# Optimization experiments

Hardware: AMD Instinct MI355X
Metric: run time of the kernel (lower is better)

The kernel has to match this reference:

```python
import jax, jax.numpy as jnp
import numpy as np
import math

B, T, D = 4, 2048, 1024
N, D_OUT = 1024, 1024
EPS_A = 1e-4
PROJ_BOUND = 1.0


def setup_inputs() -> dict:
    key = jax.random.key(0)
    ks = jax.random.split(key, 4)
    # reset_parameters: rho=0.99, delta0=1.0
    rho, delta0 = 0.99, 1.0
    alpha0 = -math.log(rho) / delta0
    alpha_log_val = math.log(math.expm1(alpha0))
    delta_bias_val = math.log(math.expm1(delta0))
    return {
        "u": jax.random.normal(ks[0], (B, T, D), dtype=jnp.float32),
        "z0": jnp.zeros((B, N), dtype=jnp.float32),
        "W_in_raw": 0.02 * jax.random.normal(ks[1], (N, D), dtype=jnp.float32),
        "W_out_raw": 0.02 * jax.random.normal(ks[2], (D_OUT, N), dtype=jnp.float32),
        "pn_w": 0.02 * jax.random.normal(ks[3], (3 * N, D), dtype=jnp.float32),
        "pn_b": jnp.zeros((3 * N,), dtype=jnp.float32),
        "alpha_log": jnp.full((N,), alpha_log_val, dtype=jnp.float32),
        "delta_bias": jnp.full((N,), delta_bias_val, dtype=jnp.float32),
        "log_gamma": jnp.float32(0.0),
    }


def _bounded_linear(x, W, bound):
    # y = x @ (W/scale)^T with ||W/scale||_2 <= bound (exact spectral norm)
    sigma = jnp.maximum(jnp.linalg.norm(W, ord=2), 1e-5)
    scale = jnp.maximum(sigma / bound, 1.0)
    return x @ (W / scale).T


def reference(u, z0, W_in_raw, W_out_raw, pn_w, pn_b, alpha_log, delta_bias, log_gamma):
    g = jnp.exp(log_gamma)
    u_scaled = g * _bounded_linear(u, W_in_raw, PROJ_BOUND)        # (B,T,N)
    raw = u @ pn_w.T + pn_b                                        # (B,T,3N)
    delta_raw, b_raw, c_raw = jnp.split(raw, 3, axis=-1)
    delta = jax.nn.softplus(delta_raw + delta_bias)
    alpha = jax.nn.softplus(alpha_log)                             # (N,)
    a = jnp.minimum(jnp.exp(-delta * alpha), 1.0 - EPS_A)          # (B,T,N)
    b = jnp.tanh(b_raw)
    c = jnp.tanh(c_raw)
    # exact spectral norm of [[a,b],[c,0]] per coordinate
    p = a * a + c * c
    r = b * b
    q = a * b
    disc = (p - r) * (p - r) + 4.0 * q * q
    lam_max = 0.5 * (p + r + jnp.sqrt(disc + 1e-12))
    sigma = jnp.sqrt(lam_max + 1e-12)
    scale = jnp.maximum(sigma, 1.0)
    a, b, c = a / scale, b / scale, c / scale
    # diagonal recurrence z_{t+1} = a_t * z_t + b_t * u_scaled_t via associative scan
    bu = b * u_scaled
    bu = bu.at[:, 0].add(a[:, 0] * z0)
    def combine(x, y):
        a1, b1 = x
        a2, b2 = y
        return (a2 * a1, a2 * b1 + b2)
    _, z_next = jax.lax.associative_scan(combine, (a, bu), axis=1)  # z_1..z_T (B,T,N)
    # y_t = W_out (c_t * z_t) with z_t = state BEFORE update (one-step delay)
    states = jnp.concatenate([z0[:, None, :], z_next[:, :-1, :]], axis=1)  # z_0..z_{T-1}
    y_hat = c * states
    y = _bounded_linear(y_hat, W_out_raw, PROJ_BOUND)              # (B,T,D_out)
    return y
```

## Files before the change

### kernel.cpp

```cpp
#include <hip/hip_runtime.h>
#include <stdint.h>

#define B_ 4
#define T_ 2048
#define D_ 1024
#define N_ 1024
#define TC 16
#define NCH (T_/TC)
#define SQN 6

typedef __attribute__((ext_vector_type(4))) float f32x4;
typedef __attribute__((ext_vector_type(8))) short bf16x8;
typedef __attribute__((ext_vector_type(4))) unsigned short us4;

__device__ __forceinline__ unsigned short f2bf(float f){
  unsigned int u = __float_as_uint(f);
  return (unsigned short)((u + 0x7fffu + ((u >> 16) & 1u)) >> 16);
}
__device__ __forceinline__ float bf2f(unsigned short h){
  return __uint_as_float(((unsigned int)h) << 16);
}

__device__ __forceinline__ float inv_scale(const float* __restrict__ sc, int z){
  float ll = 0.f, w = 1.f, t = 1.f;
  #pragma unroll
  for (int i = 0; i <= SQN; i++){
    t = sc[8 + 2*i + z];
    ll += w * __logf(t);
    w *= 0.5f;
  }
  float F = sc[8 + 2*(SQN+1) + z];
  ll += w * __logf(F / (t*t));
  float sig = fmaxf(__expf(0.5f * ll), 1e-5f);
  return 1.f / fmaxf(sig, 1.f);
}

#define U4    2097152
#define WIN4   262144
#define PNW4   786432
#define WOUT4  262144
#define CONV_BLOCKS ((U4 + WIN4 + PNW4 + WOUT4 + 255)/256)

__global__ void k_convert_all(const float* __restrict__ u, const float* __restrict__ Win,
                              const float* __restrict__ pnw, const float* __restrict__ Wout,
                              unsigned short* __restrict__ u16, unsigned short* __restrict__ Wcat16,
                              unsigned short* __restrict__ Wout16, float* __restrict__ sc){
  if (blockIdx.x == 0 && threadIdx.x < 64) sc[threadIdx.x] = 0.f;
  long i = (long)blockIdx.x * 256 + threadIdx.x;
  const float* src; long o; size_t didx; unsigned short* dbuf;
  if (i < U4){
    src = u; o = i; dbuf = u16; didx = (size_t)o;
  } else if (i < U4+WIN4){
    o = i - U4; src = Win;
    int n = (int)(o >> 8), c4 = (int)(o & 255);
    dbuf = Wcat16; didx = (size_t)(4*n)*256 + c4;
  } else if (i < U4+WIN4+PNW4){
    o = i - (U4+WIN4); src = pnw;
    int m = (int)(o >> 8), c4 = (int)(o & 255);
    int s = (m >> 10) + 1, n = m & 1023;
    dbuf = Wcat16; didx = (size_t)(4*n + s)*256 + c4;
  } else if (i < U4+WIN4+PNW4+WOUT4){
    o = i - (U4+WIN4+PNW4); src = Wout; dbuf = Wout16; didx = (size_t)o;
  } else return;
  float4 v = ((const float4*)src)[o];
  us4 w;
  w.x = f2bf(v.x); w.y = f2bf(v.y); w.z = f2bf(v.z); w.w = f2bf(v.w);
  ((us4*)dbuf)[didx] = w;
}

__device__ __forceinline__ void load_lds16(const unsigned short* g, unsigned short* l){
  __builtin_amdgcn_global_load_lds((const __attribute__((address_space(1))) void*)g,
                                   (__attribute__((address_space(3))) void*)l, 16, 0, 0);
}

template<int OUTBF16>
__global__ __launch_bounds__(256) void k_gemm(
    const unsigned short* __restrict__ A,
    const unsigned short* __restrict__ Bmat,
    void* __restrict__ C0,
    int M, int N, int K,
    const float* __restrict__ sc, int step)
{
  __shared__ alignas(16) unsigned short As[128*64];
  __shared__ alignas(16) unsigned short Bs[128*64];
  const int tid = threadIdx.x;
  const int wid = tid >> 6;
  const int lane = tid & 63;
  const int bn = blockIdx.x, bm = blockIdx.y;

  char* C = (char*)C0;
  float outscale = (step >= 0) ? inv_scale(sc, step) : 1.f;

  const int wr = wid >> 1, wc = wid & 1;
  const int rg = lane >> 3;
  const int cby = (lane & 7) << 4;
  const int srow0 = wid * 32;
  const int frow = lane & 15;
  const int kgrp = lane >> 4;

  const unsigned short* ap[4];
  const unsigned short* bp[4];
  unsigned short* adst[4];
  unsigned short* bdst[4];
  #pragma unroll
  for (int i = 0; i < 4; i++){
    int r = srow0 + i*8 + rg;
    int cb = cby ^ ((r & 7) << 4);
    ap[i] = A    + (size_t)(bm*128 + r)*K + (cb >> 1);
    bp[i] = Bmat + (size_t)(bn*128 + r)*K + (cb >> 1);
    adst[i] = As + (srow0 + i*8)*64;
    bdst[i] = Bs + (srow0 + i*8)*64;
  }

  int aoff[4][2], boff[4][2];
  #pragma unroll
  for (int m = 0; m < 4; m++){
    int r = wr*64 + m*16 + frow;
    #pragma unroll
    for (int kk = 0; kk < 2; kk++)
      aoff[m][kk] = r*128 + ((kk*64 + kgrp*16) ^ ((r & 7) << 4));
  }
  #pragma unroll
  for (int n2 = 0; n2 < 4; n2++){
    int r = wc*64 + n2*16 + frow;
    #pragma unroll
    for (int kk = 0; kk < 2; kk++)
      boff[n2][kk] = r*128 + ((kk*64 + kgrp*16) ^ ((r & 7) << 4));
  }

  f32x4 acc[4][4] = {};

  for (int kt = 0; kt < K; kt += 64){
    #pragma unroll
    for (int i = 0; i < 4; i++){
      load_lds16(ap[i], adst[i]);
      load_lds16(bp[i], bdst[i]);
      ap[i] += 64; bp[i] += 64;
    }
    __syncthreads();
    #pragma unroll
    for (int kk = 0; kk < 2; kk++){
      bf16x8 af[4], bfv[4];
      #pragma unroll
      for (int m = 0; m < 4; m++)
        af[m] = *(const bf16x8*)((const char*)As + aoff[m][kk]);
      #pragma unroll
      for (int n2 = 0; n2 < 4; n2++)
        bfv[n2] = *(const bf16x8*)((const char*)Bs + boff[n2][kk]);
      #pragma unroll
      for (int m = 0; m < 4; m++)
        #pragma unroll
        for (int n2 = 0; n2 < 4; n2++)
          acc[m][n2] = __builtin_amdgcn_mfma_f32_16x16x32_bf16(af[m], bfv[n2], acc[m][n2], 0, 0, 0);
    }
    __syncthreads();
  }

  const int row0 = bm*128 + wr*64;
  const int col0 = bn*128 + wc*64 + frow;
  #pragma unroll
  for (int m = 0; m < 4; m++){
    #pragma unroll
    for (int n2 = 0; n2 < 4; n2++){
      const int col = col0 + n2*16;
      const int rb = row0 + m*16 + kgrp*4;
      #pragma unroll
      for (int j = 0; j < 4; j++){
        float v = acc[m][n2][j] * outscale;
        if (OUTBF16) ((unsigned short*)C)[(size_t)(rb + j)*N + col] = f2bf(v);
        else         ((float*)C)[(size_t)(rb + j)*N + col] = v;
      }
    }
  }
}

__global__ __launch_bounds__(256) void k_sq(
    const unsigned short* __restrict__ A0, unsigned short* __restrict__ C0,
    const unsigned short* __restrict__ A1, unsigned short* __restrict__ C1,
    float* __restrict__ sc, int step)
{
  __shared__ alignas(16) unsigned short As0[64*128], Bs0[64*128];
  __shared__ alignas(16) unsigned short As1[64*128], Bs1[64*128];
  const int tid = threadIdx.x;
  const int wid = tid >> 6;
  const int lane = tid & 63;
  const int z = blockIdx.z;

  int x = blockIdx.x, bm = 0;
  while (x >= 16 - bm){ x -= 16 - bm; bm++; }
  const int bn = bm + x;

  const unsigned short* A = z ? A1 : A0;
  unsigned short* C = z ? C1 : C0;
  const size_t rs = (step == 0 && z == 0) ? 4096 : 1024;
  float outscale = 1.f;
  if (step > 0){ float t = sc[8 + (step-1)*2 + z]; outscale = 1.f/(t*t); }

  const int wr = wid >> 1, wc = wid & 1;
  const int frow = lane & 15;
  const int kgrp = lane >> 4;

  const int srl = lane >> 4;
  const int sgr = lane & 15;
  const int swzr = wid*4 + srl;
  const int scol_e = ((sgr ^ swzr) << 3);

  const size_t Arow = (size_t)bm * 64;
  const size_t Brow = (size_t)bn * 64;

  f32x4 acc[2][2] = {};

  auto stage = [&](unsigned short* as, unsigned short* bs, int t){
    const int kt = t * 128;
    #pragma unroll
    for (int i = 0; i < 4; i++){
      int r = i*16 + wid*4 + srl;
      load_lds16(A + (Arow + r)*rs + kt + scol_e, as + (i*16 + wid*4)*128);
      load_lds16(A + (Brow + r)*rs + kt + scol_e, bs + (i*16 + wid*4)*128);
    }
  };

  auto compute = [&](const unsigned short* as, const unsigned short* bs){
    #pragma unroll
    for (int ks = 0; ks < 4; ks++){
      const int kb = ks*64 + kgrp*16;
      bf16x8 af[2], bfv[2];
      #pragma unroll
      for (int m = 0; m < 2; m++){
        int r = wr*32 + m*16 + frow;
        af[m] = *(const bf16x8*)((const char*)as + r*256 + (kb ^ (frow << 4)));
      }
      #pragma unroll
      for (int n2 = 0; n2 < 2; n2++){
        int r = wc*32 + n2*16 + frow;
        bfv[n2] = *(const bf16x8*)((const char*)bs + r*256 + (kb ^ (frow << 4)));
      }
      #pragma unroll
      for (int m = 0; m < 2; m++)
        #pragma unroll
        for (int n2 = 0; n2 < 2; n2++)
          acc[m][n2] = __builtin_amdgcn_mfma_f32_16x16x32_bf16(af[m], bfv[n2], acc[m][n2], 0, 0, 0);
    }
  };

  stage(As0, Bs0, 0);
  __syncthreads();
  for (int t2 = 0; t2 < 8; t2 += 2){
    if (t2 + 1 < 8) stage(As1, Bs1, t2 + 1);
    compute(As0, Bs0);
    __syncthreads();
    if (t2 + 2 < 8) stage(As0, Bs0, t2 + 2);
    compute(As1, Bs1);
    __syncthreads();
  }

  const int row0 = bm*64 + wr*32;
  const int col0 = bn*64 + wc*32 + frow;
  float fr = 0.f;
  #pragma unroll
  for (int m = 0; m < 2; m++){
    #pragma unroll
    for (int n2 = 0; n2 < 2; n2++){
      const int col = col0 + n2*16;
      const int rb = row0 + m*16 + kgrp*4;
      us4 tw;
      #pragma unroll
      for (int j = 0; j < 4; j++){
        float v = acc[m][n2][j] * outscale;
        unsigned short h = f2bf(v);
        C[(size_t)(rb + j)*1024 + col] = h;
        tw[j] = h;
        fr += v*v;
      }
      if (bm != bn)
        *(us4*)(C + (size_t)col*1024 + rb) = tw;
    }
  }
  if (bm == bn && wr == wc){
    int j = frow - kgrp*4;
    if (j >= 0 && j < 4){
      float d = (acc[0][0][j] + acc[1][1][j]) * outscale;
      atomicAdd(&sc[8 + step*2 + z], d);
    }
  }
  if (step == SQN){
    if (bm != bn) fr *= 2.f;
    #pragma unroll
    for (int off = 32; off; off >>= 1) fr += __shfl_down(fr, off, 64);
    if (lane == 0) atomicAdd(&sc[8 + 2*(SQN+1) + z], fr);
  }
}

__device__ __forceinline__ float softplusf(float x){
  return (x > 0.f) ? (x + __logf(1.f + __expf(-x))) : __logf(1.f + __expf(x));
}
__device__ __forceinline__ float tanhfastf(float x){
  float e = __expf(2.f * x);
  return 1.f - 2.f/(e + 1.f);
}
__device__ __forceinline__ void abc_from(float pin, float draw, float braw, float craw,
    float alpha, float ginv, float& a_o, float& bu_o, float& c_o){
  float sp = softplusf(draw);
  float av = __expf(-sp * alpha);
  av = fminf(av, 1.f - 1e-4f);
  float bv = tanhfastf(braw);
  float cv = tanhfastf(craw);
  float p = av*av + cv*cv;
  float r = bv*bv;
  float q = av*bv;
  float pr = p - r;
  float disc = pr*pr + 4.f*q*q;
  float lam = 0.5f*(p + r + sqrtf(disc + 1e-12f));
  float inv = fminf(rsqrtf(lam + 1e-12f), 1.f);
  a_o = av * inv;
  c_o = cv * inv;
  bu_o = (bv * inv) * (pin * ginv);
}

__global__ __launch_bounds__(256) void k_pass1(
    const unsigned short* __restrict__ P,
    const float* __restrict__ alog, const float* __restrict__ dbias,
    const float* __restrict__ pnb, const float* __restrict__ lgam,
    const float* __restrict__ sc,
    float* __restrict__ Asum, float* __restrict__ Ssum)
{
  const int tid = threadIdx.x;
  const int n0 = tid*4;
  const int ch = blockIdx.x, b = blockIdx.y;
  const float ginv = __expf(lgam[0]) * inv_scale(sc, 0);
  float alpha[4], bd[4], bb[4], bc[4], A[4], S[4];
  #pragma unroll
  for (int j = 0; j < 4; j++){
    alpha[j] = softplusf(alog[n0+j]);
    bd[j] = dbias[n0+j] + pnb[n0+j];
    bb[j] = pnb[N_ + n0+j];
    bc[j] = pnb[2*N_ + n0+j];
    A[j] = 1.f; S[j] = 0.f;
  }
  const unsigned short* Pr = P + (size_t)(b*T_ + ch*TC) * 4096 + 4*n0;
  #pragma unroll 2
  for (int i = 0; i < TC; i++){
    bf16x8 e0 = *(const bf16x8*)Pr;
    bf16x8 e1 = *(const bf16x8*)(Pr + 8);
    #pragma unroll
    for (int j = 0; j < 4; j++){
      const bf16x8& e = (j < 2) ? e0 : e1;
      const int o = (j & 1)*4;
      float a, bu, c;
      abc_from(bf2f((unsigned short)e[o]),   bf2f((unsigned short)e[o+1]) + bd[j],
               bf2f((unsigned short)e[o+2]) + bb[j], bf2f((unsigned short)e[o+3]) + bc[j],
               alpha[j], ginv, a, bu, c);
      S[j] = fmaf(a, S[j], bu);
      A[j] *= a;
    }
    Pr += 4096;
  }
  const size_t idx = (size_t)(b*NCH + ch)*N_ + n0;
  #pragma unroll
  for (int j = 0; j < 4; j++){ Asum[idx+j] = A[j]; Ssum[idx+j] = S[j]; }
}

__global__ void k_pass2(const float* __restrict__ Asum, const float* __restrict__ Ssum,
                        const float* __restrict__ z0, float* __restrict__ Zent)
{
  const int n = blockIdx.x*256 + threadIdx.x;
  const int b = blockIdx.y;
  float z = z0[b*N_ + n];
  for (int ch = 0; ch < NCH; ch++){
    const size_t idx = (size_t)(b*NCH + ch)*N_ + n;
    Zent[idx] = z;
    z = fmaf(Asum[idx], z, Ssum[idx]);
  }
}

__global__ __launch_bounds__(256) void k_pass3(
    const unsigned short* __restrict__ P,
    const float* __restrict__ alog, const float* __restrict__ dbias,
    const float* __restrict__ pnb, const float* __restrict__ lgam,
    const float* __restrict__ sc, const float* __restrict__ Zent,
    unsigned short* __restrict__ yh)
{
  const int tid = threadIdx.x;
  const int n0 = tid*4;
  const int ch = blockIdx.x, b = blockIdx.y;
  const float ginv = __expf(lgam[0]) * inv_scale(sc, 0);
  float alpha[4], bd[4], bb[4], bc[4], z[4];
  #pragma unroll
  for (int j = 0; j < 4; j++){
    alpha[j] = softplusf(alog[n0+j]);
    bd[j] = dbias[n0+j] + pnb[n0+j];
    bb[j] = pnb[N_ + n0+j];
    bc[j] = pnb[2*N_ + n0+j];
  }
  const size_t zidx = (size_t)(b*NCH + ch)*N_ + n0;
  #pragma unroll
  for (int j = 0; j < 4; j++) z[j] = Zent[zidx+j];
  const unsigned short* Pr = P + (size_t)(b*T_ + ch*TC) * 4096 + 4*n0;
  unsigned short* Y = yh + (size_t)(b*T_ + ch*TC)*N_ + n0;
  #pragma unroll 2
  for (int i = 0; i < TC; i++){
    bf16x8 e0 = *(const bf16x8*)Pr;
    bf16x8 e1 = *(const bf16x8*)(Pr + 8);
    us4 ow;
    #pragma unroll
    for (int j = 0; j < 4; j++){
      const bf16x8& e = (j < 2) ? e0 : e1;
      const int o = (j & 1)*4;
      float a, bu, c;
      abc_from(bf2f((unsigned short)e[o]),   bf2f((unsigned short)e[o+1]) + bd[j],
               bf2f((unsigned short)e[o+2]) + bb[j], bf2f((unsigned short)e[o+3]) + bc[j],
               alpha[j], ginv, a, bu, c);
      float yv = c * z[j];
      z[j] = fmaf(a, z[j], bu);
      ow[j] = f2bf(yv);
    }
    *(us4*)Y = ow;
    Y += N_;
    Pr += 4096;
  }
}

extern "C" void kernel_launch(void* const* d_in, const int* in_sizes, int n_in,
                              void* d_out, int out_size, void* d_ws, size_t ws_size,
                              hipStream_t stream)
{
  const float* u    = (const float*)d_in[0];
  const float* z0   = (const float*)d_in[1];
  const float* Win  = (const float*)d_in[2];
  const float* Wout = (const float*)d_in[3];
  const float* pnw  = (const float*)d_in[4];
  const float* pnb  = (const float*)d_in[5];
  const float* alog = (const float*)d_in[6];
  const float* dbias= (const float*)d_in[7];
  const float* lgam = (const float*)d_in[8];

  char* ws = (char*)d_ws;
  size_t off = 0;
  auto alloc = [&](size_t bytes) -> void* {
    void* p = ws + off;
    off += (bytes + 255) & ~(size_t)255;
    return p;
  };
  float*          sc     = (float*)         alloc(1024);
  unsigned short* u16    = (unsigned short*)alloc((size_t)8192*1024*2);
  unsigned short* Wcat16 = (unsigned short*)alloc((size_t)4096*1024*2);
  unsigned short* Wout16 = (unsigned short*)alloc((size_t)1024*1024*2);
  unsigned short* P16    = (unsigned short*)alloc((size_t)8192*4096*2);
  unsigned short* yh16   = (unsigned short*)alloc((size_t)8192*1024*2);
  unsigned short* Hping  = (unsigned short*)alloc((size_t)2*1024*1024*2);
  unsigned short* Hpong  = (unsigned short*)alloc((size_t)2*1024*1024*2);
  float*          Asum   = (float*)alloc((size_t)B_*NCH*N_*4);
  float*          Ssum   = (float*)alloc((size_t)B_*NCH*N_*4);
  float*          Zent   = (float*)alloc((size_t)B_*NCH*N_*4);

  k_convert_all<<<CONV_BLOCKS, 256, 0, stream>>>(u, Win, pnw, Wout, u16, Wcat16, Wout16, sc);

  dim3 gsq(136, 1, 2);
  k_sq<<<gsq, 256, 0, stream>>>(Wcat16, Hping, Wout16, Hping + (size_t)1024*1024, sc, 0);
  unsigned short* hin = Hping;
  unsigned short* hout = Hpong;
  for (int s = 1; s <= SQN; s++){
    k_sq<<<gsq, 256, 0, stream>>>(hin, hout, hin + (size_t)1024*1024, hout + (size_t)1024*1024, sc, s);
    unsigned short* t = hin; hin = hout; hout = t;
  }

  dim3 g1(4096/128, 8192/128);
  k_gemm<1><<<g1, 256, 0, stream>>>(u16, Wcat16, P16, 8192, 4096, 1024, sc, -1);

  dim3 gp1(NCH, B_);
  k_pass1<<<gp1, 256, 0, stream>>>(P16, alog, dbias, pnb, lgam, sc, Asum, Ssum);
  dim3 gp2(N_/256, B_);
  k_pass2<<<gp2, 256, 0, stream>>>(Asum, Ssum, z0, Zent);
  k_pass3<<<gp1, 256, 0, stream>>>(P16, alog, dbias, pnb, lgam, sc, Zent, yh16);

  dim3 g2(1024/128, 8192/128);
  k_gemm<0><<<g2, 256, 0, stream>>>(yh16, Wout16, d_out, 8192, 1024, 1024, sc, 1);
}
```

Before: 290.6 us.

## Fuse gate nonlinearity and chunk scan summaries into projection GEMM epilogue

The projection GEMM epilogue now transposes MFMA accumulators with lane shuffles, computes a, b·u and c per element, and stores packed bf16 a/c plus fp32 bu. It also reduces 16-step chunk summaries (A, S) with cross-lane shuffles. The separate pass1/pass2/pass3 kernels become a single scan kernel that folds all earlier chunk summaries serially per chunk and then runs the recurrence. This removes the bf16 P intermediate being read twice and the repeated transcendental work, in exchange for a heavier GEMM epilogue and an O(NCH) prefix loop per block.

Result: no change. 290.3 us (-0.1%).

```diff
diff --git a/kernel.cpp b/kernel.cpp
--- a/kernel.cpp
+++ b/kernel.cpp
@@ -33,6 +33,32 @@
   ll += w * __logf(F / (t*t));
   float sig = fmaxf(__expf(0.5f * ll), 1e-5f);
   return 1.f / fmaxf(sig, 1.f);
+}
+
+__device__ __forceinline__ float softplusf(float x){
+  return (x > 0.f) ? (x + __logf(1.f + __expf(-x))) : __logf(1.f + __expf(x));
+}
+__device__ __forceinline__ float tanhfastf(float x){
+  float e = __expf(2.f * x);
+  return 1.f - 2.f/(e + 1.f);
+}
+__device__ __forceinline__ void abc_from(float pin, float draw, float braw, float craw,
+    float alpha, float ginv, float& a_o, float& bu_o, float& c_o){
+  float sp = softplusf(draw);
+  float av = __expf(-sp * alpha);
+  av = fminf(av, 1.f - 1e-4f);
+  float bv = tanhfastf(braw);
+  float cv = tanhfastf(craw);
+  float p = av*av + cv*cv;
+  float r = bv*bv;
+  float q = av*bv;
+  float pr = p - r;
+  float disc = pr*pr + 4.f*q*q;
+  float lam = 0.5f*(p + r + sqrtf(disc + 1e-12f));
+  float inv = fminf(rsqrtf(lam + 1e-12f), 1.f);
+  a_o = av * inv;
+  c_o = cv * inv;
+  bu_o = (bv * inv) * (pin * ginv);
 }
 
 #define U4    2097152
@@ -73,11 +99,140 @@
                                    (__attribute__((address_space(3))) void*)l, 16, 0, 0);
 }
 
-template<int OUTBF16>
+__global__ __launch_bounds__(256) void k_pgemm(
+    const unsigned short* __restrict__ A,
+    const unsigned short* __restrict__ Bmat,
+    const float* __restrict__ alog, const float* __restrict__ dbias,
+    const float* __restrict__ pnb, const float* __restrict__ lgam,
+    const float* __restrict__ sc,
+    unsigned int* __restrict__ G1,
+    float* __restrict__ G2,
+    float* __restrict__ Asum, float* __restrict__ Ssum)
+{
+  __shared__ alignas(16) unsigned short As[128*64];
+  __shared__ alignas(16) unsigned short Bs[128*64];
+  const int tid = threadIdx.x;
+  const int wid = tid >> 6;
+  const int lane = tid & 63;
+  const int bn = blockIdx.x, bm = blockIdx.y;
+  const int K = 1024;
+
+  const int wr = wid >> 1, wc = wid & 1;
+  const int rg = lane >> 3;
+  const int cby = (lane & 7) << 4;
+  const int srow0 = wid * 32;
+  const int frow = lane & 15;
+  const int kgrp = lane >> 4;
+
+  const unsigned short* ap[4];
+  const unsigned short* bp[4];
+  unsigned short* adst[4];
+  unsigned short* bdst[4];
+  #pragma unroll
+  for (int i = 0; i < 4; i++){
+    int r = srow0 + i*8 + rg;
+    int cb = cby ^ ((r & 7) << 4);
+    ap[i] = A    + (size_t)(bm*128 + r)*K + (cb >> 1);
+    bp[i] = Bmat + (size_t)(bn*128 + r)*K + (cb >> 1);
+    adst[i] = As + (srow0 + i*8)*64;
+    bdst[i] = Bs + (srow0 + i*8)*64;
+  }
+  int aoff[4][2], boff[4][2];
+  #pragma unroll
+  for (int m = 0; m < 4; m++){
+    int r = wr*64 + m*16 + frow;
+    #pragma unroll
+    for (int kk = 0; kk < 2; kk++)
+      aoff[m][kk] = r*128 + ((kk*64 + kgrp*16) ^ ((r & 7) << 4));
+  }
+  #pragma unroll
+  for (int n2 = 0; n2 < 4; n2++){
+    int r = wc*64 + n2*16 + frow;
+    #pragma unroll
+    for (int kk = 0; kk < 2; kk++)
+      boff[n2][kk] = r*128 + ((kk*64 + kgrp*16) ^ ((r & 7) << 4));
+  }
+
+  f32x4 acc[4][4] = {};
+
+  for (int kt = 0; kt < K; kt += 64){
+    #pragma unroll
+    for (int i = 0; i < 4; i++){
+      load_lds16(ap[i], adst[i]);
+      load_lds16(bp[i], bdst[i]);
+      ap[i] += 64; bp[i] += 64;
+    }
+    __syncthreads();
+    #pragma unroll
+    for (int kk = 0; kk < 2; kk++){
+      bf16x8 af[4], bfv[4];
+      #pragma unroll
+      for (int m = 0; m < 4; m++)
+        af[m] = *(const bf16x8*)((const char*)As + aoff[m][kk]);
+      #pragma unroll
+      for (int n2 = 0; n2 < 4; n2++)
+        bfv[n2] = *(const bf16x8*)((const char*)Bs + boff[n2][kk]);
+      #pragma unroll
+      for (int m = 0; m < 4; m++)
+        #pragma unroll
+        for (int n2 = 0; n2 < 4; n2++)
+          acc[m][n2] = __builtin_amdgcn_mfma_f32_16x16x32_bf16(af[m], bfv[n2], acc[m][n2], 0, 0, 0);
+    }
+    __syncthreads();
+  }
+
+  const int q = (lane >> 2) & 3;
+  const int s = lane & 3;
+  const bool sb0 = (lane & 1) != 0;
+  const bool sb1 = (lane & 2) != 0;
+  const float ginv = __expf(lgam[0]) * inv_scale(sc, 0);
+
+  float alpP[4], bdP[4], bbP[4], bcP[4];
+  #pragma unroll
+  for (int n2 = 0; n2 < 4; n2++){
+    int n = bn*32 + wc*16 + n2*4 + q;
+    alpP[n2] = softplusf(alog[n]);
+    bdP[n2] = dbias[n] + pnb[n];
+    bbP[n2] = pnb[N_ + n];
+    bcP[n2] = pnb[2*N_ + n];
+  }
+
+  #pragma unroll
+  for (int m = 0; m < 4; m++){
+    #pragma unroll
+    for (int n2 = 0; n2 < 4; n2++){
+      f32x4 v = acc[m][n2];
+      { float x = sb0 ? v[0] : v[1]; float y = __shfl_xor(x, 1, 64); if (sb0) v[0] = y; else v[1] = y; }
+      { float x = sb0 ? v[2] : v[3]; float y = __shfl_xor(x, 1, 64); if (sb0) v[2] = y; else v[3] = y; }
+      { float x = sb1 ? v[0] : v[2]; float y = __shfl_xor(x, 2, 64); if (sb1) v[0] = y; else v[2] = y; }
+      { float x = sb1 ? v[1] : v[3]; float y = __shfl_xor(x, 2, 64); if (sb1) v[1] = y; else v[3] = y; }
+      float a, bu, c;
+      abc_from(v[0], v[1] + bdP[n2], v[2] + bbP[n2], v[3] + bcP[n2], alpP[n2], ginv, a, bu, c);
+      const int row = bm*128 + wr*64 + m*16 + kgrp*4 + s;
+      const int n = bn*32 + wc*16 + n2*4 + q;
+      G1[(size_t)row*N_ + n] = (unsigned int)f2bf(a) | ((unsigned int)f2bf(c) << 16);
+      G2[(size_t)row*N_ + n] = bu;
+      float Ar = a, Sr = bu;
+      { float Ap = __shfl_xor(Ar,1,64), Sp = __shfl_xor(Sr,1,64);
+        if (lane & 1){ Sr = fmaf(Ar, Sp, Sr); } else { Sr = fmaf(Ap, Sr, Sp); } Ar *= Ap; }
+      { float Ap = __shfl_xor(Ar,2,64), Sp = __shfl_xor(Sr,2,64);
+        if (lane & 2){ Sr = fmaf(Ar, Sp, Sr); } else { Sr = fmaf(Ap, Sr, Sp); } Ar *= Ap; }
+      { float Ap = __shfl_xor(Ar,16,64), Sp = __shfl_xor(Sr,16,64);
+        if (lane & 16){ Sr = fmaf(Ar, Sp, Sr); } else { Sr = fmaf(Ap, Sr, Sp); } Ar *= Ap; }
+      { float Ap = __shfl_xor(Ar,32,64), Sp = __shfl_xor(Sr,32,64);
+        if (lane & 32){ Sr = fmaf(Ar, Sp, Sr); } else { Sr = fmaf(Ap, Sr, Sp); } Ar *= Ap; }
+      if ((lane & 0x33) == 0){
+        const size_t ci = (size_t)(row >> 4)*N_ + n;
+        Asum[ci] = Ar; Ssum[ci] = Sr;
+      }
+    }
+  }
+}
+
 __global__ __launch_bounds__(256) void k_gemm(
     const unsigned short* __restrict__ A,
     const unsigned short* __restrict__ Bmat,
-    void* __restrict__ C0,
+    float* __restrict__ C,
     int M, int N, int K,
     const float* __restrict__ sc, int step)
 {
@@ -88,7 +243,6 @@
   const int lane = tid & 63;
   const int bn = blockIdx.x, bm = blockIdx.y;
 
-  char* C = (char*)C0;
   float outscale = (step >= 0) ? inv_scale(sc, step) : 1.f;
 
   const int wr = wid >> 1, wc = wid & 1;
@@ -111,7 +265,6 @@
     adst[i] = As + (srow0 + i*8)*64;
     bdst[i] = Bs + (srow0 + i*8)*64;
   }
-
   int aoff[4][2], boff[4][2];
   #pragma unroll
   for (int m = 0; m < 4; m++){
@@ -165,11 +318,8 @@
       const int col = col0 + n2*16;
       const int rb = row0 + m*16 + kgrp*4;
       #pragma unroll
-      for (int j = 0; j < 4; j++){
-        float v = acc[m][n2][j] * outscale;
-        if (OUTBF16) ((unsigned short*)C)[(size_t)(rb + j)*N + col] = f2bf(v);
-        else         ((float*)C)[(size_t)(rb + j)*N + col] = v;
-      }
+      for (int j = 0; j < 4; j++)
+        C[(size_t)(rb + j)*N + col] = acc[m][n2][j] * outscale;
     }
   }
 }
@@ -291,132 +441,47 @@
   }
 }
 
-__device__ __forceinline__ float softplusf(float x){
-  return (x > 0.f) ? (x + __logf(1.f + __expf(-x))) : __logf(1.f + __expf(x));
-}
-__device__ __forceinline__ float tanhfastf(float x){
-  float e = __expf(2.f * x);
-  return 1.f - 2.f/(e + 1.f);
-}
-__device__ __forceinline__ void abc_from(float pin, float draw, float braw, float craw,
-    float alpha, float ginv, float& a_o, float& bu_o, float& c_o){
-  float sp = softplusf(draw);
-  float av = __expf(-sp * alpha);
-  av = fminf(av, 1.f - 1e-4f);
-  float bv = tanhfastf(braw);
-  float cv = tanhfastf(craw);
-  float p = av*av + cv*cv;
-  float r = bv*bv;
-  float q = av*bv;
-  float pr = p - r;
-  float disc = pr*pr + 4.f*q*q;
-  float lam = 0.5f*(p + r + sqrtf(disc + 1e-12f));
-  float inv = fminf(rsqrtf(lam + 1e-12f), 1.f);
-  a_o = av * inv;
-  c_o = cv * inv;
-  bu_o = (bv * inv) * (pin * ginv);
-}
-
-__global__ __launch_bounds__(256) void k_pass1(
-    const unsigned short* __restrict__ P,
-    const float* __restrict__ alog, const float* __restrict__ dbias,
-    const float* __restrict__ pnb, const float* __restrict__ lgam,
-    const float* __restrict__ sc,
-    float* __restrict__ Asum, float* __restrict__ Ssum)
+__global__ __launch_bounds__(256) void k_scan(
+    const unsigned int* __restrict__ G1, const float* __restrict__ G2,
+    const float* __restrict__ Asum, const float* __restrict__ Ssum,
+    const float* __restrict__ z0, unsigned short* __restrict__ yh)
 {
   const int tid = threadIdx.x;
   const int n0 = tid*4;
   const int ch = blockIdx.x, b = blockIdx.y;
-  const float ginv = __expf(lgam[0]) * inv_scale(sc, 0);
-  float alpha[4], bd[4], bb[4], bc[4], A[4], S[4];
-  #pragma unroll
-  for (int j = 0; j < 4; j++){
-    alpha[j] = softplusf(alog[n0+j]);
-    bd[j] = dbias[n0+j] + pnb[n0+j];
-    bb[j] = pnb[N_ + n0+j];
-    bc[j] = pnb[2*N_ + n0+j];
-    A[j] = 1.f; S[j] = 0.f;
-  }
-  const unsigned short* Pr = P + (size_t)(b*T_ + ch*TC) * 4096 + 4*n0;
-  #pragma unroll 2
+  float z[4];
+  #pragma unroll
+  for (int j = 0; j < 4; j++) z[j] = z0[b*N_ + n0 + j];
+  for (int c2 = 0; c2 < ch; c2++){
+    const size_t idx = (size_t)(b*NCH + c2)*N_ + n0;
+    float4 Av = *(const float4*)(Asum + idx);
+    float4 Sv = *(const float4*)(Ssum + idx);
+    z[0] = fmaf(Av.x, z[0], Sv.x);
+    z[1] = fmaf(Av.y, z[1], Sv.y);
+    z[2] = fmaf(Av.z, z[2], Sv.z);
+    z[3] = fmaf(Av.w, z[3], Sv.w);
+  }
+  const size_t base = (size_t)(b*T_ + ch*TC)*N_ + n0;
+  const unsigned int* g1 = G1 + base;
+  const float* g2 = G2 + base;
+  unsigned short* Y = yh + base;
+  #pragma unroll 4
   for (int i = 0; i < TC; i++){
-    bf16x8 e0 = *(const bf16x8*)Pr;
-    bf16x8 e1 = *(const bf16x8*)(Pr + 8);
+    uint4 pac = *(const uint4*)g1;
+    float4 bu = *(const float4*)g2;
+    us4 ow;
     #pragma unroll
     for (int j = 0; j < 4; j++){
-      const bf16x8& e = (j < 2) ? e0 : e1;
-      const int o = (j & 1)*4;
-      float a, bu, c;
-      abc_from(bf2f((unsigned short)e[o]),   bf2f((unsigned short)e[o+1]) + bd[j],
-               bf2f((unsigned short)e[o+2]) + bb[j], bf2f((unsigned short)e[o+3]) + bc[j],
-               alpha[j], ginv, a, bu, c);
-      S[j] = fmaf(a, S[j], bu);
-      A[j] *= a;
-    }
-    Pr += 4096;
-  }
-  const size_t idx = (size_t)(b*NCH + ch)*N_ + n0;
-  #pragma unroll
-  for (int j = 0; j < 4; j++){ Asum[idx+j] = A[j]; Ssum[idx+j] = S[j]; }
-}
-
-__global__ void k_pass2(const float* __restrict__ Asum, const float* __restrict__ Ssum,
-                        const float* __restrict__ z0, float* __restrict__ Zent)
-{
-  const int n = blockIdx.x*256 + threadIdx.x;
-  const int b = blockIdx.y;
-  float z = z0[b*N_ + n];
-  for (int ch = 0; ch < NCH; ch++){
-    const size_t idx = (size_t)(b*NCH + ch)*N_ + n;
-    Zent[idx] = z;
-    z = fmaf(Asum[idx], z, Ssum[idx]);
-  }
-}
-
-__global__ __launch_bounds__(256) void k_pass3(
-    const unsigned short* __restrict__ P,
-    const float* __restrict__ alog, const float* __restrict__ dbias,
-    const float* __restrict__ pnb, const float* __restrict__ lgam,
-    const float* __restrict__ sc, const float* __restrict__ Zent,
-    unsigned short* __restrict__ yh)
-{
-  const int tid = threadIdx.x;
-  const int n0 = tid*4;
-  const int ch = blockIdx.x, b = blockIdx.y;
-  const float ginv = __expf(lgam[0]) * inv_scale(sc, 0);
-  float alpha[4], bd[4], bb[4], bc[4], z[4];
-  #pragma unroll
-  for (int j = 0; j < 4; j++){
-    alpha[j] = softplusf(alog[n0+j]);
-    bd[j] = dbias[n0+j] + pnb[n0+j];
-    bb[j] = pnb[N_ + n0+j];
-    bc[j] = pnb[2*N_ + n0+j];
-  }
-  const size_t zidx = (size_t)(b*NCH + ch)*N_ + n0;
-  #pragma unroll
-  for (int j = 0; j < 4; j++) z[j] = Zent[zidx+j];
-  const unsigned short* Pr = P + (size_t)(b*T_ + ch*TC) * 4096 + 4*n0;
-  unsigned short* Y = yh + (size_t)(b*T_ + ch*TC)*N_ + n0;
-  #pragma unroll 2
-  for (int i = 0; i < TC; i++){
-    bf16x8 e0 = *(const bf16x8*)Pr;
-    bf16x8 e1 = *(const bf16x8*)(Pr + 8);
-    us4 ow;
-    #pragma unroll
-    for (int j = 0; j < 4; j++){
-      const bf16x8& e = (j < 2) ? e0 : e1;
-      const int o = (j & 1)*4;
-      float a, bu, c;
-      abc_from(bf2f((unsigned short)e[o]),   bf2f((unsigned short)e[o+1]) + bd[j],
-               bf2f((unsigned short)e[o+2]) + bb[j], bf2f((unsigned short)e[o+3]) + bc[j],
-               alpha[j], ginv, a, bu, c);
+      unsigned int p = j==0 ? pac.x : j==1 ? pac.y : j==2 ? pac.z : pac.w;
+      float buj     = j==0 ? bu.x  : j==1 ? bu.y  : j==2 ? bu.z  : bu.w;
+      float a = bf2f((unsigned short)(p & 0xffffu));
+      float c = bf2f((unsigned short)(p >> 16));
       float yv = c * z[j];
-      z[j] = fmaf(a, z[j], bu);
+      z[j] = fmaf(a, z[j], buj);
       ow[j] = f2bf(yv);
     }
     *(us4*)Y = ow;
-    Y += N_;
-    Pr += 4096;
+    g1 += N_; g2 += N_; Y += N_;
   }
 }
 
@@ -445,13 +510,13 @@
   unsigned short* u16    = (unsigned short*)alloc((size_t)8192*1024*2);
   unsigned short* Wcat16 = (unsigned short*)alloc((size_t)4096*1024*2);
   unsigned short* Wout16 = (unsigned short*)alloc((size_t)1024*1024*2);
-  unsigned short* P16    = (unsigned short*)alloc((size_t)8192*4096*2);
+  unsigned int*   G1     = (unsigned int*)  alloc((size_t)8192*1024*4);
+  float*          G2     = (float*)         alloc((size_t)8192*1024*4);
   unsigned short* yh16   = (unsigned short*)alloc((size_t)8192*1024*2);
   unsigned short* Hping  = (unsigned short*)alloc((size_t)2*1024*1024*2);
   unsigned short* Hpong  = (unsigned short*)alloc((size_t)2*1024*1024*2);
   float*          Asum   = (float*)alloc((size_t)B_*NCH*N_*4);
   float*          Ssum   = (float*)alloc((size_t)B_*NCH*N_*4);
-  float*          Zent   = (float*)alloc((size_t)B_*NCH*N_*4);
 
   k_convert_all<<<CONV_BLOCKS, 256, 0, stream>>>(u, Win, pnw, Wout, u16, Wcat16, Wout16, sc);
 
@@ -465,14 +530,12 @@
   }
 
   dim3 g1(4096/128, 8192/128);
-  k_gemm<1><<<g1, 256, 0, stream>>>(u16, Wcat16, P16, 8192, 4096, 1024, sc, -1);
-
-  dim3 gp1(NCH, B_);
-  k_pass1<<<gp1, 256, 0, stream>>>(P16, alog, dbias, pnb, lgam, sc, Asum, Ssum);
-  dim3 gp2(N_/256, B_);
-  k_pass2<<<gp2, 256, 0, stream>>>(Asum, Ssum, z0, Zent);
-  k_pass3<<<gp1, 256, 0, stream>>>(P16, alog, dbias, pnb, lgam, sc, Zent, yh16);
+  k_pgemm<<<g1, 256, 0, stream>>>(u16, Wcat16, alog, dbias, pnb, lgam, sc, G1, G2, Asum, Ssum);
+
+  dim3 gsc(NCH, B_);
+  k_scan<<<gsc, 256, 0, stream>>>(G1, G2, Asum, Ssum, z0, yh16);
 
   dim3 g2(1024/128, 8192/128);
-  k_gemm<0><<<g2, 256, 0, stream>>>(yh16, Wout16, d_out, 8192, 1024, 1024, sc, 1);
-}
+  k_gemm<<<g2, 256, 0, stream>>>(yh16, Wout16, d_out == nullptr ? nullptr : (float*)d_out,
+                                 8192, 1024, 1024, sc, 1);
+}
```

## Fold chunk-prefix scan into pass3 and halve per-thread work in scan kernels

Applied to the files above, without the earlier changes.

Removes the serial pass2 kernel by having each pass3 block recompute its chunk entry state, walking all preceding chunk summaries (Asum/Ssum) itself. This eliminates one launch and the Zent buffer, but adds redundant O(ch) sequential loads per block, up to 127 steps. Pass1 and pass3 now give each thread 2 channels instead of 4 and use twice as many blocks, which raises occupancy and parallelism in the memory-bound scan phases.

Result: slower. 306.9 us (+5.6%).

```diff
diff --git a/kernel.cpp b/kernel.cpp
--- a/kernel.cpp
+++ b/kernel.cpp
@@ -33,6 +33,32 @@
   ll += w * __logf(F / (t*t));
   float sig = fmaxf(__expf(0.5f * ll), 1e-5f);
   return 1.f / fmaxf(sig, 1.f);
+}
+
+__device__ __forceinline__ float softplusf(float x){
+  return (x > 0.f) ? (x + __logf(1.f + __expf(-x))) : __logf(1.f + __expf(x));
+}
+__device__ __forceinline__ float tanhfastf(float x){
+  float e = __expf(2.f * x);
+  return 1.f - 2.f/(e + 1.f);
+}
+__device__ __forceinline__ void abc_from(float pin, float draw, float braw, float craw,
+    float alpha, float ginv, float& a_o, float& bu_o, float& c_o){
+  float sp = softplusf(draw);
+  float av = __expf(-sp * alpha);
+  av = fminf(av, 1.f - 1e-4f);
+  float bv = tanhfastf(braw);
+  float cv = tanhfastf(craw);
+  float p = av*av + cv*cv;
+  float r = bv*bv;
+  float q = av*bv;
+  float pr = p - r;
+  float disc = pr*pr + 4.f*q*q;
+  float lam = 0.5f*(p + r + sqrtf(disc + 1e-12f));
+  float inv = fminf(rsqrtf(lam + 1e-12f), 1.f);
+  a_o = av * inv;
+  c_o = cv * inv;
+  bu_o = (bv * inv) * (pin * ginv);
 }
 
 #define U4    2097152
@@ -111,7 +137,6 @@
     adst[i] = As + (srow0 + i*8)*64;
     bdst[i] = Bs + (srow0 + i*8)*64;
   }
-
   int aoff[4][2], boff[4][2];
   #pragma unroll
   for (int m = 0; m < 4; m++){
@@ -291,33 +316,7 @@
   }
 }
 
-__device__ __forceinline__ float softplusf(float x){
-  return (x > 0.f) ? (x + __logf(1.f + __expf(-x))) : __logf(1.f + __expf(x));
-}
-__device__ __forceinline__ float tanhfastf(float x){
-  float e = __expf(2.f * x);
-  return 1.f - 2.f/(e + 1.f);
-}
-__device__ __forceinline__ void abc_from(float pin, float draw, float braw, float craw,
-    float alpha, float ginv, float& a_o, float& bu_o, float& c_o){
-  float sp = softplusf(draw);
-  float av = __expf(-sp * alpha);
-  av = fminf(av, 1.f - 1e-4f);
-  float bv = tanhfastf(braw);
-  float cv = tanhfastf(craw);
-  float p = av*av + cv*cv;
-  float r = bv*bv;
-  float q = av*bv;
-  float pr = p - r;
-  float disc = pr*pr + 4.f*q*q;
-  float lam = 0.5f*(p + r + sqrtf(disc + 1e-12f));
-  float inv = fminf(rsqrtf(lam + 1e-12f), 1.f);
-  a_o = av * inv;
-  c_o = cv * inv;
-  bu_o = (bv * inv) * (pin * ginv);
-}
-
-__global__ __launch_bounds__(256) void k_pass1(
+__global__ __launch_bounds__(256) void k_gate(
     const unsigned short* __restrict__ P,
     const float* __restrict__ alog, const float* __restrict__ dbias,
     const float* __restrict__ pnb, const float* __restrict__ lgam,
@@ -325,27 +324,24 @@
     float* __restrict__ Asum, float* __restrict__ Ssum)
 {
   const int tid = threadIdx.x;
-  const int n0 = tid*4;
-  const int ch = blockIdx.x, b = blockIdx.y;
+  const int n0 = blockIdx.y*512 + tid*2;
+  const int ch = blockIdx.x, b = blockIdx.z;
   const float ginv = __expf(lgam[0]) * inv_scale(sc, 0);
-  float alpha[4], bd[4], bb[4], bc[4], A[4], S[4];
-  #pragma unroll
-  for (int j = 0; j < 4; j++){
+  float alpha[2], bd[2], bb[2], bc[2], A[2] = {1.f,1.f}, S[2] = {0.f,0.f};
+  #pragma unroll
+  for (int j = 0; j < 2; j++){
     alpha[j] = softplusf(alog[n0+j]);
     bd[j] = dbias[n0+j] + pnb[n0+j];
     bb[j] = pnb[N_ + n0+j];
     bc[j] = pnb[2*N_ + n0+j];
-    A[j] = 1.f; S[j] = 0.f;
-  }
-  const unsigned short* Pr = P + (size_t)(b*T_ + ch*TC) * 4096 + 4*n0;
-  #pragma unroll 2
+  }
+  const unsigned short* Pr = P + (size_t)(b*T_ + ch*TC)*4096 + 4*n0;
+  #pragma unroll 4
   for (int i = 0; i < TC; i++){
-    bf16x8 e0 = *(const bf16x8*)Pr;
-    bf16x8 e1 = *(const bf16x8*)(Pr + 8);
-    #pragma unroll
-    for (int j = 0; j < 4; j++){
-      const bf16x8& e = (j < 2) ? e0 : e1;
-      const int o = (j & 1)*4;
+    bf16x8 e = *(const bf16x8*)Pr;
+    #pragma unroll
+    for (int j = 0; j < 2; j++){
+      const int o = j*4;
       float a, bu, c;
       abc_from(bf2f((unsigned short)e[o]),   bf2f((unsigned short)e[o+1]) + bd[j],
                bf2f((unsigned short)e[o+2]) + bb[j], bf2f((unsigned short)e[o+3]) + bc[j],
@@ -356,65 +352,56 @@
     Pr += 4096;
   }
   const size_t idx = (size_t)(b*NCH + ch)*N_ + n0;
-  #pragma unroll
-  for (int j = 0; j < 4; j++){ Asum[idx+j] = A[j]; Ssum[idx+j] = S[j]; }
-}
-
-__global__ void k_pass2(const float* __restrict__ Asum, const float* __restrict__ Ssum,
-                        const float* __restrict__ z0, float* __restrict__ Zent)
-{
-  const int n = blockIdx.x*256 + threadIdx.x;
-  const int b = blockIdx.y;
-  float z = z0[b*N_ + n];
-  for (int ch = 0; ch < NCH; ch++){
-    const size_t idx = (size_t)(b*NCH + ch)*N_ + n;
-    Zent[idx] = z;
-    z = fmaf(Asum[idx], z, Ssum[idx]);
-  }
-}
-
-__global__ __launch_bounds__(256) void k_pass3(
+  Asum[idx] = A[0]; Asum[idx+1] = A[1];
+  Ssum[idx] = S[0]; Ssum[idx+1] = S[1];
+}
+
+__global__ __launch_bounds__(256) void k_scan3(
     const unsigned short* __restrict__ P,
     const float* __restrict__ alog, const float* __restrict__ dbias,
     const float* __restrict__ pnb, const float* __restrict__ lgam,
-    const float* __restrict__ sc, const float* __restrict__ Zent,
-    unsigned short* __restrict__ yh)
+    const float* __restrict__ sc,
+    const float* __restrict__ Asum, const float* __restrict__ Ssum,
+    const float* __restrict__ z0, unsigned short* __restrict__ yh)
 {
   const int tid = threadIdx.x;
-  const int n0 = tid*4;
-  const int ch = blockIdx.x, b = blockIdx.y;
+  const int n0 = blockIdx.y*512 + tid*2;
+  const int ch = blockIdx.x, b = blockIdx.z;
   const float ginv = __expf(lgam[0]) * inv_scale(sc, 0);
-  float alpha[4], bd[4], bb[4], bc[4], z[4];
-  #pragma unroll
-  for (int j = 0; j < 4; j++){
+  float alpha[2], bd[2], bb[2], bc[2], z[2];
+  #pragma unroll
+  for (int j = 0; j < 2; j++){
     alpha[j] = softplusf(alog[n0+j]);
     bd[j] = dbias[n0+j] + pnb[n0+j];
     bb[j] = pnb[N_ + n0+j];
     bc[j] = pnb[2*N_ + n0+j];
-  }
-  const size_t zidx = (size_t)(b*NCH + ch)*N_ + n0;
-  #pragma unroll
-  for (int j = 0; j < 4; j++) z[j] = Zent[zidx+j];
-  const unsigned short* Pr = P + (size_t)(b*T_ + ch*TC) * 4096 + 4*n0;
+    z[j] = z0[b*N_ + n0 + j];
+  }
+  for (int c2 = 0; c2 < ch; c2++){
+    const size_t idx = (size_t)(b*NCH + c2)*N_ + n0;
+    float2 Av = *(const float2*)(Asum + idx);
+    float2 Sv = *(const float2*)(Ssum + idx);
+    z[0] = fmaf(Av.x, z[0], Sv.x);
+    z[1] = fmaf(Av.y, z[1], Sv.y);
+  }
+  const unsigned short* Pr = P + (size_t)(b*T_ + ch*TC)*4096 + 4*n0;
   unsigned short* Y = yh + (size_t)(b*T_ + ch*TC)*N_ + n0;
-  #pragma unroll 2
+  #pragma unroll 4
   for (int i = 0; i < TC; i++){
-    bf16x8 e0 = *(const bf16x8*)Pr;
-    bf16x8 e1 = *(const bf16x8*)(Pr + 8);
-    us4 ow;
-    #pragma unroll
-    for (int j = 0; j < 4; j++){
-      const bf16x8& e = (j < 2) ? e0 : e1;
-      const int o = (j & 1)*4;
+    bf16x8 e = *(const bf16x8*)Pr;
+    unsigned int ow = 0;
+    #pragma unroll
+    for (int j = 0; j < 2; j++){
+      const int o = j*4;
       float a, bu, c;
       abc_from(bf2f((unsigned short)e[o]),   bf2f((unsigned short)e[o+1]) + bd[j],
                bf2f((unsigned short)e[o+2]) + bb[j], bf2f((unsigned short)e[o+3]) + bc[j],
                alpha[j], ginv, a, bu, c);
       float yv = c * z[j];
       z[j] = fmaf(a, z[j], bu);
-      ow[j] = f2bf(yv);
-    }
-    *(us4*)Y = ow;
+      ow |= ((unsigned int)f2bf(yv)) << (16*j);
+    }
+    *(unsigned int*)Y = ow;
     Y += N_;
     Pr += 4096;
   }
@@ -451,7 +438,6 @@
   unsigned short* Hpong  = (unsigned short*)alloc((size_t)2*1024*1024*2);
   float*          Asum   = (float*)alloc((size_t)B_*NCH*N_*4);
   float*          Ssum   = (float*)alloc((size_t)B_*NCH*N_*4);
-  float*          Zent   = (float*)alloc((size_t)B_*NCH*N_*4);
 
   k_convert_all<<<CONV_BLOCKS, 256, 0, stream>>>(u, Win, pnw, Wout, u16, Wcat16, Wout16, sc);
 
@@ -467,11 +453,10 @@
   dim3 g1(4096/128, 8192/128);
   k_gemm<1><<<g1, 256, 0, stream>>>(u16, Wcat16, P16, 8192, 4096, 1024, sc, -1);
 
-  dim3 gp1(NCH, B_);
-  k_pass1<<<gp1, 256, 0, stream>>>(P16, alog, dbias, pnb, lgam, sc, Asum, Ssum);
-  dim3 gp2(N_/256, B_);
-  k_pass2<<<gp2, 256, 0, stream>>>(Asum, Ssum, z0, Zent);
-  k_pass3<<<gp1, 256, 0, stream>>>(P16, alog, dbias, pnb, lgam, sc, Zent, yh16);
+  dim3 gg(NCH, 2, B_);
+  k_gate<<<gg, 256, 0, stream>>>(P16, alog, dbias, pnb, lgam, sc, Asum, Ssum);
+
+  k_scan3<<<gg, 256, 0, stream>>>(P16, alog, dbias, pnb, lgam, sc, Asum, Ssum, z0, yh16);
 
   dim3 g2(1024/128, 8192/128);
   k_gemm<0><<<g2, 256, 0, stream>>>(yh16, Wout16, d_out, 8192, 1024, 1024, sc, 1);
```
